# Kernel tuning notes

Measured on AMD Instinct MI355X. Metric: run time of the kernel, lower is better.

Reference implementation:

```python
import jax, jax.numpy as jnp
import numpy as np
import math

B, S, H, E, TOPK, NHEADS = 8, 512, 1024, 8, 2, 8
CAP = int(B * S * 1.5 * TOPK / E)  # 1536


def _linear(x, w, b):
    # torch nn.Linear convention: y = x @ w.T + b, w: [out, in]
    return x @ w.T + b


def _mha(x, in_w, in_b, out_w, out_b, n_heads):
    # torch nn.MultiheadAttention self-attention, eval mode (no dropout)
    Bx, Sx, D = x.shape
    dh = D // n_heads
    qkv = x @ in_w.T + in_b                      # [B,S,3D]
    q, k, v = jnp.split(qkv, 3, axis=-1)
    def heads(t):
        return t.reshape(Bx, Sx, n_heads, dh).transpose(0, 2, 1, 3)  # [B,h,S,dh]
    q, k, v = heads(q), heads(k), heads(v)
    scores = jnp.einsum('bhqd,bhkd->bhqk', q, k) / math.sqrt(dh)
    attn = jax.nn.softmax(scores, axis=-1)
    o = jnp.einsum('bhqk,bhkd->bhqd', attn, v)   # [B,h,S,dh]
    o = o.transpose(0, 2, 1, 3).reshape(Bx, Sx, D)
    return o @ out_w.T + out_b


def setup_inputs() -> dict:
    key = jax.random.key(0)
    ks = jax.random.split(key, 24)
    sc = 0.02
    d = {
        'hidden_states': jax.random.normal(ks[0], (B, S, H), jnp.float32),
        'pos_emb': jax.random.normal(ks[1], (S, H), jnp.float32) * sc,
        'se_w1': jax.random.normal(ks[2], (H // 4, 1), jnp.float32) * sc,
        'se_b1': jnp.zeros((H // 4,), jnp.float32),
        'se_w2': jax.random.normal(ks[3], (H // 4, H // 4), jnp.float32) * sc,
        'se_b2': jnp.zeros((H // 4,), jnp.float32),
        'sexp_w': jax.random.normal(ks[4], (H, H // 4), jnp.float32) * sc,
        'sexp_b': jnp.zeros((H,), jnp.float32),
        'te_w1': jax.random.normal(ks[5], (H, H + 2), jnp.float32) * sc,
        'te_b1': jnp.zeros((H,), jnp.float32),
        'te_w2': jax.random.normal(ks[6], (H, H), jnp.float32) * sc,
        'te_b2': jnp.zeros((H,), jnp.float32),
        'attn_in_w': jax.random.normal(ks[7], (3 * H, H), jnp.float32) * sc,
        'attn_in_b': jnp.zeros((3 * H,), jnp.float32),
        'attn_out_w': jax.random.normal(ks[8], (H, H), jnp.float32) * sc,
        'attn_out_b': jnp.zeros((H,), jnp.float32),
        'tr_w1': jax.random.normal(ks[9], (H, H), jnp.float32) * sc,
        'tr_b1': jnp.zeros((H,), jnp.float32),
        'tr_w2': jax.random.normal(ks[10], (E, H), jnp.float32) * sc,
        'tr_b2': jnp.zeros((E,), jnp.float32),
    }
    return d


def reference(hidden_states, pos_emb, se_w1, se_b1, se_w2, se_b2, sexp_w, sexp_b,
              te_w1, te_b1, te_w2, te_b2, attn_in_w, attn_in_b, attn_out_w, attn_out_b,
              tr_w1, tr_b1, tr_w2, tr_b2):
    b, s, h = hidden_states.shape
    timestamps = jnp.arange(s, dtype=hidden_states.dtype)           # [S]
    seasonality = jnp.sin(timestamps * 2 * jnp.pi / 24)             # [S]
    ts_b = jnp.broadcast_to(timestamps, (b, s))
    se_b = jnp.broadcast_to(seasonality, (b, s))

    position_embeddings = pos_emb[:s][None]                          # [1,S,H]
    seas = jax.nn.relu(_linear(se_b[..., None], se_w1, se_b1))       # [B,S,H/4]
    seas = _linear(seas, se_w2, se_b2)
    seasonal_embeddings = _linear(seas, sexp_w, sexp_b)              # [B,S,H]

    time_features = jnp.stack([ts_b, se_b], axis=-1)                 # [B,S,2]
    combined = jnp.concatenate([hidden_states, time_features], -1)   # [B,S,H+2]
    enc = jax.nn.relu(_linear(combined, te_w1, te_b1))
    enc = _linear(enc, te_w2, te_b2)
    enc = enc + position_embeddings + seasonal_embeddings
    enc = _mha(enc, attn_in_w, attn_in_b, attn_out_w, attn_out_b, NHEADS)

    logits = _linear(jax.nn.relu(_linear(enc, tr_w1, tr_b1)), tr_w2, tr_b2)  # [B,S,E]
    router_probs = jax.nn.softmax(logits, axis=-1)
    top_k_probs, top_k_idx = jax.lax.top_k(router_probs, TOPK)
    top_k_probs = top_k_probs / top_k_probs.sum(-1, keepdims=True)

    capacity = int(b * s * 1.5 * TOPK / E)
    # top-k indices are distinct per token, so summed one-hots replicate the
    # python loop's slot-0 writes exactly.
    onehot = jax.nn.one_hot(top_k_idx, E, dtype=router_probs.dtype)  # [B,S,K,E]
    disp0 = onehot.sum(axis=2)                                        # [B,S,E]
    comb0 = jnp.einsum('bske,bsk->bse', onehot, top_k_probs)          # [B,S,E]
    dispatch = jnp.zeros((b, s, E, capacity), router_probs.dtype).at[:, :, :, 0].set(disp0)
    combine = jnp.zeros((b, s, E, capacity), router_probs.dtype).at[:, :, :, 0].set(comb0)

    p_mean = router_probs.mean(axis=(0, 1))
    aux_loss = jnp.sum(p_mean * jnp.log(p_mean * E + 1e-9))
    return dispatch, combine, router_probs, aux_loss
```

## Files before the change

### kernel.cpp

```cpp
#include <hip/hip_runtime.h>
#include <hip/hip_bf16.h>


#define Hh 1024

typedef __attribute__((ext_vector_type(8))) short short8v;
typedef __attribute__((ext_vector_type(4))) float f32x4;

static __device__ __forceinline__ ushort f2bf(float x) {
  uint u = __float_as_uint(x);
  u += 0x7FFF + ((u >> 16) & 1);
  return (ushort)(u >> 16);
}
static __device__ __forceinline__ float bf2f(ushort h) {
  return __uint_as_float(((uint)h) << 16);
}

template<int EPI, bool RELU, bool HAS_BN, bool HAS_BSN>
__global__ __launch_bounds__(256, 2) void mgemm_k(
    const ushort* __restrict__ A, int lda, long long sAmaj, long long sAmin, int aHi, int aLo,
    const ushort* __restrict__ Bf, int BNT, int BKC, long long sBmaj, long long sBmin,
    float* __restrict__ Cf, ushort* __restrict__ Ch, int ldc, long long sCmaj, long long sCmin,
    int splitOff,
    ushort* __restrict__ pK, ushort* __restrict__ pV,
    int Kd, int zdiv,
    const float* __restrict__ bN, const float* __restrict__ bSN, int ldbs, int smod,
    float alpha)
{
  int gx = gridDim.x, gy = gridDim.y;
  int lin = (blockIdx.z * gy + blockIdx.y) * gx + blockIdx.x;
  int nwg = gx * gy * gridDim.z;
  int cpx = nwg >> 3;
  int swz = (lin & 7) * cpx + (lin >> 3);
  int bz = swz / (gx * gy);
  int rem = swz - bz * (gx * gy);
  int by = rem / gx, bx = rem - by * gx;

  int zj = bz / zdiv, zi = bz - zj * zdiv;
  A += (size_t)zj * sAmaj + (size_t)zi * sAmin;
  const ushort* bfb = Bf + (size_t)zj * sBmaj + (size_t)zi * sBmin;
  long long coff = (long long)zj * sCmaj + (long long)zi * sCmin;

  int m0 = by * 128, n0 = bx * 128;

  __shared__ __align__(16) ushort smem[16384];

  int t = threadIdx.x;
  int l = t & 63, w = t >> 6;
  int wm = w >> 1, wn = w & 1;

  f32x4 acc[4][4];
#pragma unroll
  for (int i = 0; i < 4; ++i)
#pragma unroll
    for (int j = 0; j < 4; ++j) acc[i][j] = (f32x4){0.f, 0.f, 0.f, 0.f};

  int srow = t >> 1;
  int sc = (t & 1) * 2;
  const ushort* gAh = A + (size_t)(m0 + srow) * lda + aHi + sc * 8;
  const ushort* gAl = A + (size_t)(m0 + srow) * lda + aLo + sc * 8;
  int wsw = ((srow >> 1) & 7) << 4;
  int wo0 = (srow * 64 + sc * 16) ^ wsw;
  int wo1 = wo0 ^ 16;

  int aoff[4];
#pragma unroll
  for (int mi = 0; mi < 4; ++mi) {
    int row = wm * 64 + mi * 16 + (l & 15);
    aoff[mi] = (row * 64 + (l >> 4) * 16) ^ (((row >> 1) & 7) << 4);
  }

  const ushort* bph[4];
  const ushort* bpl[4];
  int ntg0 = (n0 >> 4) + wn * 4;
#pragma unroll
  for (int ni = 0; ni < 4; ++ni) {
    bph[ni] = bfb + ((size_t)(ntg0 + ni) * BKC) * 512 + l * 8;
    bpl[ni] = bfb + ((size_t)(BNT + ntg0 + ni) * BKC) * 512 + l * 8;
  }

  int4 a0h0, a0h1, a0l0, a0l1, a1h0, a1h1, a1l0, a1l1;
  short8v B0h[4], B0l[4], B1h[4], B1l[4];

#define LOADA0(s) { a0h0 = *(const int4*)(gAh + (s)*32); a0h1 = *(const int4*)(gAh + (s)*32 + 8); \
                    a0l0 = *(const int4*)(gAl + (s)*32); a0l1 = *(const int4*)(gAl + (s)*32 + 8); }
#define LOADA1(s) { a1h0 = *(const int4*)(gAh + (s)*32); a1h1 = *(const int4*)(gAh + (s)*32 + 8); \
                    a1l0 = *(const int4*)(gAl + (s)*32); a1l1 = *(const int4*)(gAl + (s)*32 + 8); }
#define STOREA(h0, h1, l0, l1, base) { char* nb = (char*)smem + (base); \
    *(int4*)(nb + wo0) = h0; *(int4*)(nb + wo1) = h1; \
    *(int4*)(nb + 8192 + wo0) = l0; *(int4*)(nb + 8192 + wo1) = l1; }
#define LOADB(BH, BL, s) { _Pragma("unroll") \
    for (int ni = 0; ni < 4; ++ni) { \
      BH[ni] = *(const short8v*)(bph[ni] + (size_t)(s) * 512); \
      BL[ni] = *(const short8v*)(bpl[ni] + (size_t)(s) * 512); } }
#define MFMA_STEP(ahb, alb, BH, BL) { \
    short8v ah[4], al[4]; \
    _Pragma("unroll") for (int mi = 0; mi < 4; ++mi) \
      ah[mi] = *(const short8v*)((char*)smem + (ahb) + aoff[mi]); \
    _Pragma("unroll") for (int mi = 0; mi < 4; ++mi) \
      al[mi] = *(const short8v*)((char*)smem + (alb) + aoff[mi]); \
    _Pragma("unroll") for (int ni = 0; ni < 4; ++ni) \
      _Pragma("unroll") for (int mi = 0; mi < 4; ++mi) \
        acc[mi][ni] = __builtin_amdgcn_mfma_f32_16x16x32_bf16(ah[mi], BH[ni], acc[mi][ni], 0, 0, 0); \
    _Pragma("unroll") for (int ni = 0; ni < 4; ++ni) \
      _Pragma("unroll") for (int mi = 0; mi < 4; ++mi) \
        acc[mi][ni] = __builtin_amdgcn_mfma_f32_16x16x32_bf16(al[mi], BH[ni], acc[mi][ni], 0, 0, 0); \
    _Pragma("unroll") for (int ni = 0; ni < 4; ++ni) \
      _Pragma("unroll") for (int mi = 0; mi < 4; ++mi) \
        acc[mi][ni] = __builtin_amdgcn_mfma_f32_16x16x32_bf16(ah[mi], BL[ni], acc[mi][ni], 0, 0, 0); }

  int nt = Kd >> 5;
  LOADA0(0); LOADB(B0h, B0l, 0);
  LOADA1(1); LOADB(B1h, B1l, 1);
  STOREA(a0h0, a0h1, a0l0, a0l1, 0);
  __syncthreads();
  for (int s2 = 0; s2 < nt; s2 += 2) {
    if (s2 + 2 < nt) LOADA0(s2 + 2);
    MFMA_STEP(0, 8192, B0h, B0l);
    if (s2 + 2 < nt) LOADB(B0h, B0l, s2 + 2);
    STOREA(a1h0, a1h1, a1l0, a1l1, 16384);
    __syncthreads();
    if (s2 + 3 < nt) LOADA1(s2 + 3);
    MFMA_STEP(16384, 24576, B1h, B1l);
    if (s2 + 3 < nt) LOADB(B1h, B1l, s2 + 3);
    if (s2 + 2 < nt) STOREA(a0h0, a0h1, a0l0, a0l1, 0);
    __syncthreads();
  }
#undef LOADA0
#undef LOADA1
#undef STOREA
#undef LOADB
#undef MFMA_STEP

#pragma unroll
  for (int mi = 0; mi < 4; ++mi)
#pragma unroll
    for (int j = 0; j < 4; ++j) {
      int m = m0 + wm * 64 + mi * 16 + (l >> 4) * 4 + j;
#pragma unroll
      for (int ni = 0; ni < 4; ++ni) {
        int n = n0 + wn * 64 + ni * 16 + (l & 15);
        float x = acc[mi][ni][j] * alpha;
        if (HAS_BN) x += bN[n];
        if (HAS_BSN) x += bSN[(size_t)(m % smod) * ldbs + n];
        if (RELU) x = fmaxf(x, 0.f);
        acc[mi][ni][j] = x;
      }
    }

  if (EPI == 0) {
    float* Fs = (float*)smem;
#pragma unroll
    for (int p = 0; p < 2; ++p) {
      __syncthreads();
      if (wm == p) {
#pragma unroll
        for (int mi = 0; mi < 4; ++mi)
#pragma unroll
          for (int j = 0; j < 4; ++j) {
            int r = mi * 16 + (l >> 4) * 4 + j;
#pragma unroll
            for (int ni = 0; ni < 4; ++ni) {
              int c = wn * 64 + ni * 16 + (l & 15);
              *(float*)((char*)Fs + ((r * 512 + c * 4) ^ ((r & 7) << 4))) = acc[mi][ni][j];
            }
          }
      }
      __syncthreads();
#pragma unroll
      for (int r8 = 0; r8 < 8; ++r8) {
        int idx = r8 * 256 + t;
        int row = idx >> 5, slot = idx & 31;
        int4 v = *(const int4*)((char*)Fs + ((row * 512 + slot * 16) ^ ((row & 7) << 4)));
        *(int4*)(Cf + coff + (size_t)(m0 + p * 64 + row) * ldc + n0 + slot * 4) = v;
      }
    }
  } else {
    __syncthreads();
    ushort* Es = smem;
    bool isQ = (EPI == 1) || (n0 < 1024);
    bool isK = (EPI == 2) && !isQ && (n0 < 2048);
    int bb = m0 >> 9, s0 = m0 & 511;
    int hh2 = isK ? ((n0 - 1024) >> 7) : ((n0 - 2048) >> 7);
    size_t kvb = (size_t)(bb * 8 + hh2) * 131072;
#pragma unroll
    for (int pass = 0; pass < 2; ++pass) {
      if (isQ) {
#pragma unroll
        for (int mi = 0; mi < 4; ++mi)
#pragma unroll
          for (int j = 0; j < 4; ++j) {
            int lr = wm * 64 + mi * 16 + (l >> 4) * 4 + j;
#pragma unroll
            for (int ni = 0; ni < 4; ++ni) {
              int lcb = (wn * 64 + ni * 16 + (l & 15)) * 2;
              float x = acc[mi][ni][j];
              ushort h = f2bf(x);
              ushort vv = (pass == 0) ? h : f2bf(x - bf2f(h));
              *(ushort*)((char*)Es + ((lr * 256 + lcb) ^ ((lr & 7) << 4))) = vv;
            }
          }
      } else if (isK) {
#pragma unroll
        for (int mi = 0; mi < 4; ++mi)
#pragma unroll
          for (int j = 0; j < 4; ++j) {
            int lr = wm * 64 + mi * 16 + (l >> 4) * 4 + j;
#pragma unroll
            for (int ni = 0; ni < 4; ++ni) {
              int lcb = (wn * 64 + ni * 16 + (l & 15)) * 2;
              float x = acc[mi][ni][j];
              ushort h = f2bf(x);
              ushort vv = (pass == 0) ? h : f2bf(x - bf2f(h));
              *(ushort*)((char*)Es + ((lr * 256 + lcb) ^ ((lr & 7) << 4))) = vv;
            }
          }
      } else {
#pragma unroll
        for (int mi = 0; mi < 4; ++mi)
#pragma unroll
          for (int j = 0; j < 4; ++j) {
            int cc = (wm * 64 + mi * 16 + (l >> 4) * 4 + j) * 2;
#pragma unroll
            for (int ni = 0; ni < 4; ++ni) {
              int rr = wn * 64 + ni * 16 + (l & 15);
              float x = acc[mi][ni][j];
              ushort h = f2bf(x);
              ushort vv = (pass == 0) ? h : f2bf(x - bf2f(h));
              *(ushort*)((char*)Es + ((rr * 256 + cc) ^ ((rr & 7) << 4))) = vv;
            }
          }
      }
      __syncthreads();
      if (isQ) {
        int off = (pass == 0) ? 0 : splitOff;
#pragma unroll
        for (int r = 0; r < 8; ++r) {
          int idx = r * 256 + t;
          int row = idx >> 4, cb = (idx & 15) * 16;
          int4 v = *(const int4*)((char*)Es + ((row * 256 + cb) ^ ((row & 7) << 4)));
          *(int4*)((char*)(Ch + coff + (size_t)(m0 + row) * ldc + off + n0) + cb) = v;
        }
      } else if (isK) {
#pragma unroll
        for (int sw = 0; sw < 8; ++sw) {
          int idx = sw * 256 + t;
          int f = idx >> 6, l2 = idx & 63;
          int st = f >> 2, dc = f & 3;
          int row = st * 16 + (l2 & 15);
          int colB = (dc * 32 + ((l2 >> 4) << 3)) * 2;
          short8v v = *(const short8v*)((char*)Es + ((row * 256 + colB) ^ ((row & 7) << 4)));
          *(short8v*)(pK + kvb + (size_t)((pass * 32 + (s0 >> 4) + st) * 4 + dc) * 512 + l2 * 8) = v;
        }
      } else {
#pragma unroll
        for (int sw = 0; sw < 8; ++sw) {
          int idx = sw * 256 + t;
          int f = idx >> 6, l2 = idx & 63;
          int dt = f >> 2, sch = f & 3;
          int row = dt * 16 + (l2 & 15);
          int colB = (sch * 32 + ((l2 >> 4) << 3)) * 2;
          short8v v = *(const short8v*)((char*)Es + ((row * 256 + colB) ^ ((row & 7) << 4)));
          *(short8v*)(pV + kvb + (size_t)((pass * 8 + dt) * 16 + (s0 >> 5) + sch) * 512 + l2 * 8) = v;
        }
      }
      if (pass == 0) __syncthreads();
    }
  }
}

__global__ __launch_bounds__(64) void convertf_k(
    const float* __restrict__ W, int ldw, ushort* __restrict__ Wf, int NT, int KC)
{
  int kc = blockIdx.x, nt2 = blockIdx.y, l = threadIdx.x;
  const float* src = W + (size_t)(nt2 * 16 + (l & 15)) * ldw + kc * 32 + ((l >> 4) << 3);
  ushort h8[8], l8[8];
#pragma unroll
  for (int j = 0; j < 8; ++j) {
    float x = src[j];
    h8[j] = f2bf(x);
    l8[j] = f2bf(x - bf2f(h8[j]));
  }
  *(int4*)(Wf + ((size_t)nt2 * KC + kc) * 512 + l * 8) = *(int4*)h8;
  *(int4*)(Wf + ((size_t)(NT + nt2) * KC + kc) * 512 + l * 8) = *(int4*)l8;
}

__global__ __launch_bounds__(256) void convert_k(
    const float* __restrict__ W, int lda, ushort* __restrict__ Whl, int K)
{
  int r = blockIdx.x;
  int c = threadIdx.x * 4;
  const float* src = W + (size_t)r * lda + c;
  float x0 = src[0], x1 = src[1], x2 = src[2], x3 = src[3];
  ushort4 h, lo;
  h.x = f2bf(x0); lo.x = f2bf(x0 - bf2f(h.x));
  h.y = f2bf(x1); lo.y = f2bf(x1 - bf2f(h.y));
  h.z = f2bf(x2); lo.z = f2bf(x2 - bf2f(h.z));
  h.w = f2bf(x3); lo.w = f2bf(x3 - bf2f(h.w));
  ushort* dst = Whl + (size_t)r * 2 * K;
  *(ushort4*)&dst[c] = h;
  *(ushort4*)&dst[K + c] = lo;
}

__global__ __launch_bounds__(256) void precompute_k(
    const float* __restrict__ pos_emb,
    const float* __restrict__ se_w1, const float* __restrict__ se_b1,
    const float* __restrict__ se_w2, const float* __restrict__ se_b2,
    const float* __restrict__ sexp_w, const float* __restrict__ sexp_b,
    const float* __restrict__ te_w1, const float* __restrict__ te_b1,
    float* __restrict__ psea, float* __restrict__ bias1)
{
  int s = blockIdx.x, t = threadIdx.x;
  float ts = (float)s;
  float se = sinf(((ts * 2.0f) * 3.14159274101257324f) / 24.0f);
  __shared__ float l1[256], l2[256];
  l1[t] = fmaxf(se * se_w1[t] + se_b1[t], 0.f);
  __syncthreads();
  {
    float a = se_b2[t];
    const float* wr = se_w2 + (size_t)t * 256;
    for (int i = 0; i < 256; ++i) a += l1[i] * wr[i];
    l2[t] = a;
  }
  __syncthreads();
#pragma unroll
  for (int r = 0; r < 4; ++r) {
    int h = r * 256 + t;
    float v = sexp_b[h];
    const float* wr = sexp_w + (size_t)h * 256;
    for (int j = 0; j < 256; ++j) v += l2[j] * wr[j];
    psea[s * Hh + h] = pos_emb[s * Hh + h] + v;
    bias1[s * Hh + h] = te_b1[h] + ts * te_w1[(size_t)h * 1026 + 1024]
                                 + se * te_w1[(size_t)h * 1026 + 1025];
  }
}

__global__ __launch_bounds__(256) void softmax2_k(float* __restrict__ S)
{
  int row = blockIdx.x * 4 + (threadIdx.x >> 6);
  int lane = threadIdx.x & 63;
  float* p = S + (size_t)row * 512;
  float4 a = *(float4*)&p[lane * 4];
  float4 b = *(float4*)&p[256 + lane * 4];
  float m = fmaxf(fmaxf(fmaxf(a.x, a.y), fmaxf(a.z, a.w)),
                  fmaxf(fmaxf(b.x, b.y), fmaxf(b.z, b.w)));
#pragma unroll
  for (int off = 32; off; off >>= 1) m = fmaxf(m, __shfl_xor(m, off));
  a.x = expf(a.x - m); a.y = expf(a.y - m); a.z = expf(a.z - m); a.w = expf(a.w - m);
  b.x = expf(b.x - m); b.y = expf(b.y - m); b.z = expf(b.z - m); b.w = expf(b.w - m);
  float s = a.x + a.y + a.z + a.w + b.x + b.y + b.z + b.w;
#pragma unroll
  for (int off = 32; off; off >>= 1) s += __shfl_xor(s, off);
  float inv = 1.f / s;
  a.x *= inv; a.y *= inv; a.z *= inv; a.w *= inv;
  b.x *= inv; b.y *= inv; b.z *= inv; b.w *= inv;
  ushort* u = (ushort*)S + (size_t)row * 1024;
  ushort4 ha, la, hb, lb;
  ha.x = f2bf(a.x); la.x = f2bf(a.x - bf2f(ha.x));
  ha.y = f2bf(a.y); la.y = f2bf(a.y - bf2f(ha.y));
  ha.z = f2bf(a.z); la.z = f2bf(a.z - bf2f(ha.z));
  ha.w = f2bf(a.w); la.w = f2bf(a.w - bf2f(ha.w));
  hb.x = f2bf(b.x); lb.x = f2bf(b.x - bf2f(hb.x));
  hb.y = f2bf(b.y); lb.y = f2bf(b.y - bf2f(hb.y));
  hb.z = f2bf(b.z); lb.z = f2bf(b.z - bf2f(hb.z));
  hb.w = f2bf(b.w); lb.w = f2bf(b.w - bf2f(hb.w));
  *(ushort4*)&u[lane * 4] = ha;
  *(ushort4*)&u[512 + lane * 4] = la;
  *(ushort4*)&u[256 + lane * 4] = hb;
  *(ushort4*)&u[768 + lane * 4] = lb;
}

__global__ __launch_bounds__(256) void tr2_k(
    const float* __restrict__ h1, const float* __restrict__ w,
    const float* __restrict__ bias, float* __restrict__ logits)
{
  int wid = threadIdx.x >> 6, lane = threadIdx.x & 63;
  int t = blockIdx.x * 4 + wid;
  const float* x = h1 + (size_t)t * Hh;
  float acc[8];
#pragma unroll
  for (int e = 0; e < 8; ++e) acc[e] = 0.f;
  for (int k = lane; k < Hh; k += 64) {
    float xv = x[k];
#pragma unroll
    for (int e = 0; e < 8; ++e) acc[e] += xv * w[e * Hh + k];
  }
#pragma unroll
  for (int e = 0; e < 8; ++e) {
#pragma unroll
    for (int off = 32; off; off >>= 1) acc[e] += __shfl_xor(acc[e], off);
  }
  if (lane == 0) {
#pragma unroll
    for (int e = 0; e < 8; ++e) logits[(size_t)t * 8 + e] = acc[e] + bias[e];
  }
}

__global__ __launch_bounds__(256) void fill0_k(float4* __restrict__ p, long long n4)
{
  long long i = (long long)blockIdx.x * 256 + threadIdx.x;
  long long stride = (long long)gridDim.x * 256;
  float4 z = make_float4(0.f, 0.f, 0.f, 0.f);
  for (; i < n4; i += stride) p[i] = z;
}

__global__ __launch_bounds__(256) void router_k(
    float* __restrict__ out, float* __restrict__ partials)
{
  int t = blockIdx.x * 256 + threadIdx.x;
  float* lg = out + 100663296 + (size_t)t * 8;
  float p[8];
#pragma unroll
  for (int e = 0; e < 8; ++e) p[e] = lg[e];
  float m = p[0];
#pragma unroll
  for (int e = 1; e < 8; ++e) m = fmaxf(m, p[e]);
  float s = 0.f;
#pragma unroll
  for (int e = 0; e < 8; ++e) { p[e] = expf(p[e] - m); s += p[e]; }
  float inv = 1.f / s;
#pragma unroll
  for (int e = 0; e < 8; ++e) p[e] *= inv;
#pragma unroll
  for (int e = 0; e < 8; ++e) lg[e] = p[e];

  int i0 = 0; float v0 = p[0];
#pragma unroll
  for (int e = 1; e < 8; ++e) if (p[e] > v0) { v0 = p[e]; i0 = e; }
  int i1 = -1; float v1 = -1.f;
#pragma unroll
  for (int e = 0; e < 8; ++e) if (e != i0 && p[e] > v1) { v1 = p[e]; i1 = e; }
  float wn = 1.f / (v0 + v1);
  size_t db = (size_t)t * (8 * 1536);
  out[db + (size_t)i0 * 1536] = 1.f;
  out[db + (size_t)i1 * 1536] = 1.f;
  out[50331648 + db + (size_t)i0 * 1536] = v0 * wn;
  out[50331648 + db + (size_t)i1 * 1536] = v1 * wn;

  __shared__ float red[256];
#pragma unroll
  for (int e = 0; e < 8; ++e) {
    red[threadIdx.x] = p[e];
    __syncthreads();
    for (int st = 128; st; st >>= 1) {
      if (threadIdx.x < st) red[threadIdx.x] += red[threadIdx.x + st];
      __syncthreads();
    }
    if (threadIdx.x == 0) partials[blockIdx.x * 8 + e] = red[0];
    __syncthreads();
  }
}

__global__ __launch_bounds__(64) void aux_k(float* __restrict__ partials,
                                            float* __restrict__ out)
{
  int lane = threadIdx.x;
  float v = 0.f;
  if (lane < 8) {
    float s = 0.f;
    for (int b = 0; b < 16; ++b) s += partials[b * 8 + lane];
    float pm = s / 4096.f;
    v = pm * logf(pm * 8.f + 1e-9f);
  }
#pragma unroll
  for (int off = 4; off; off >>= 1) v += __shfl_xor(v, off);
  if (lane == 0) out[100696064] = v;
  partials[lane] = 0.f;
  partials[64 + lane] = 0.f;
}

extern "C" void kernel_launch(void* const* d_in, const int* in_sizes, int n_in,
                              void* d_out, int out_size, void* d_ws, size_t ws_size,
                              hipStream_t stream)
{
  const float* hidden = (const float*)d_in[0];
  const float* pos_emb = (const float*)d_in[1];
  const float* se_w1 = (const float*)d_in[2];
  const float* se_b1 = (const float*)d_in[3];
  const float* se_w2 = (const float*)d_in[4];
  const float* se_b2 = (const float*)d_in[5];
  const float* sexp_w = (const float*)d_in[6];
  const float* sexp_b = (const float*)d_in[7];
  const float* te_w1 = (const float*)d_in[8];
  const float* te_b1 = (const float*)d_in[9];
  const float* te_w2 = (const float*)d_in[10];
  const float* te_b2 = (const float*)d_in[11];
  const float* ain_w = (const float*)d_in[12];
  const float* ain_b = (const float*)d_in[13];
  const float* aout_w = (const float*)d_in[14];
  const float* aout_b = (const float*)d_in[15];
  const float* tr_w1 = (const float*)d_in[16];
  const float* tr_b1 = (const float*)d_in[17];
  const float* tr_w2 = (const float*)d_in[18];
  const float* tr_b2 = (const float*)d_in[19];
  float* out = (float*)d_out;

  char* arena = (char*)d_out;
  ushort* W1f  = (ushort*)(arena + 0);
  ushort* W2f  = (ushort*)(arena + 4194304);
  ushort* Waf  = (ushort*)(arena + 8388608);
  ushort* Wof  = (ushort*)(arena + 20971520);
  ushort* Wtf  = (ushort*)(arena + 25165824);
  ushort* hid2 = (ushort*)(arena + 29360128);
  ushort* enc1 = (ushort*)(arena + 46137344);
  ushort* enc2 = (ushort*)(arena + 62914560);
  ushort* qbuf = (ushort*)(arena + 79691776);
  ushort* Kf   = (ushort*)(arena + 96468992);
  ushort* Vf   = (ushort*)(arena + 113246208);
  float*  scor = (float*)(arena + 130023424);
  ushort* attno= (ushort*)(arena + 197132288);
  ushort* encf = (ushort*)(arena + 213909504);
  float*  h1   = (float*)(arena + 230686720);
  float*  psea = (float*)(arena + 247463936);
  float*  bias1= (float*)(arena + 249561088);
  float*  parts= out + 51380224;
  float*  lgts = out + 100663296;

  convertf_k<<<dim3(32, 64), 64, 0, stream>>>(te_w1, 1026, W1f, 64, 32);
  convertf_k<<<dim3(32, 64), 64, 0, stream>>>(te_w2, 1024, W2f, 64, 32);
  convertf_k<<<dim3(32, 192), 64, 0, stream>>>(ain_w, 1024, Waf, 192, 32);
  convertf_k<<<dim3(32, 64), 64, 0, stream>>>(aout_w, 1024, Wof, 64, 32);
  convertf_k<<<dim3(32, 64), 64, 0, stream>>>(tr_w1, 1024, Wtf, 64, 32);
  convert_k<<<4096, 256, 0, stream>>>(hidden, 1024, hid2, 1024);

  precompute_k<<<512, 256, 0, stream>>>(pos_emb, se_w1, se_b1, se_w2, se_b2,
                                        sexp_w, sexp_b, te_w1, te_b1, psea, bias1);

  mgemm_k<1, true, false, true><<<dim3(8, 32, 1), 256, 0, stream>>>(
      hid2, 2048, 0, 0, 0, 1024,
      W1f, 64, 32, 0, 0,
      nullptr, enc1, 2048, 0, 0, 1024, nullptr, nullptr,
      1024, 1, nullptr, bias1, 1024, 512, 1.f);

  mgemm_k<1, false, true, true><<<dim3(8, 32, 1), 256, 0, stream>>>(
      enc1, 2048, 0, 0, 0, 1024,
      W2f, 64, 32, 0, 0,
      nullptr, enc2, 2048, 0, 0, 1024, nullptr, nullptr,
      1024, 1, te_b2, psea, 1024, 512, 1.f);

  mgemm_k<2, false, true, false><<<dim3(24, 32, 1), 256, 0, stream>>>(
      enc2, 2048, 0, 0, 0, 1024,
      Waf, 192, 32, 0, 0,
      nullptr, qbuf, 2048, 0, 0, 1024, Kf, Vf,
      1024, 1, ain_b, nullptr, 1, 1, 1.f);

  mgemm_k<0, false, false, false><<<dim3(4, 4, 64), 256, 0, stream>>>(
      qbuf, 2048, 1048576, 128, 0, 1024,
      Kf, 32, 4, 1048576, 131072,
      scor, nullptr, 512, 2097152, 262144, 0, nullptr, nullptr,
      128, 8, nullptr, nullptr, 1, 1, 0.08838834764831845f);

  softmax2_k<<<8192, 256, 0, stream>>>(scor);

  mgemm_k<1, false, false, false><<<dim3(1, 4, 64), 256, 0, stream>>>(
      (const ushort*)scor, 1024, 4194304, 524288, 0, 512,
      Vf, 8, 16, 1048576, 131072,
      nullptr, attno, 2048, 1048576, 128, 1024, nullptr, nullptr,
      512, 8, nullptr, nullptr, 1, 1, 1.f);

  mgemm_k<1, false, true, false><<<dim3(8, 32, 1), 256, 0, stream>>>(
      attno, 2048, 0, 0, 0, 1024,
      Wof, 64, 32, 0, 0,
      nullptr, encf, 2048, 0, 0, 1024, nullptr, nullptr,
      1024, 1, aout_b, nullptr, 1, 1, 1.f);

  mgemm_k<0, true, true, false><<<dim3(8, 32, 1), 256, 0, stream>>>(
      encf, 2048, 0, 0, 0, 1024,
      Wtf, 64, 32, 0, 0,
      h1, nullptr, 1024, 0, 0, 0, nullptr, nullptr,
      1024, 1, tr_b1, nullptr, 1, 1, 1.f);

  tr2_k<<<1024, 256, 0, stream>>>(h1, tr_w2, tr_b2, lgts);

  fill0_k<<<4096, 256, 0, stream>>>((float4*)out, 25165824LL);

  router_k<<<16, 256, 0, stream>>>(out, parts);
  aux_k<<<1, 64, 0, stream>>>(parts, out);
}
```

Before: 481.4 us.

## Fuse dispatch zero-fill into GEMM tails, bf16 score output, lighter barriers

Moves the zeroing of the first half of the output (the dispatch tensor region) into the tails of the early GEMM kernels, each block clearing a 128KB slice. The scratch arena is relocated into the combine region so those zero writes do not clobber live data. The fill kernel now only clears the combine half. The QK^T GEMM now writes split bf16 hi/lo scores directly, and softmax reads them, which halves score traffic and drops a float round-trip. GEMM __syncthreads are replaced with an explicit lgkmcnt wait plus s_barrier, which may relax vmem waits but relies on the correct ordering of the global loads.

```diff
diff --git a/kernel.cpp b/kernel.cpp
--- a/kernel.cpp
+++ b/kernel.cpp
@@ -15,6 +15,14 @@
 static __device__ __forceinline__ float bf2f(ushort h) {
   return __uint_as_float(((uint)h) << 16);
 }
+
+#define KBARRIER() do { \
+    __builtin_amdgcn_sched_barrier(0); \
+    asm volatile("s_waitcnt lgkmcnt(0)" ::: "memory"); \
+    __builtin_amdgcn_sched_barrier(0); \
+    __builtin_amdgcn_s_barrier(); \
+    __builtin_amdgcn_sched_barrier(0); \
+  } while (0)
 
 template<int EPI, bool RELU, bool HAS_BN, bool HAS_BSN>
 __global__ __launch_bounds__(256, 2) void mgemm_k(
@@ -25,7 +33,8 @@
     ushort* __restrict__ pK, ushort* __restrict__ pV,
     int Kd, int zdiv,
     const float* __restrict__ bN, const float* __restrict__ bSN, int ldbs, int smod,
-    float alpha)
+    float alpha,
+    char* __restrict__ zout, long long zbase, long long zlimit)
 {
   int gx = gridDim.x, gy = gridDim.y;
   int lin = (blockIdx.z * gy + blockIdx.y) * gx + blockIdx.x;
@@ -113,18 +122,18 @@
   LOADA0(0); LOADB(B0h, B0l, 0);
   LOADA1(1); LOADB(B1h, B1l, 1);
   STOREA(a0h0, a0h1, a0l0, a0l1, 0);
-  __syncthreads();
+  KBARRIER();
   for (int s2 = 0; s2 < nt; s2 += 2) {
     if (s2 + 2 < nt) LOADA0(s2 + 2);
     MFMA_STEP(0, 8192, B0h, B0l);
     if (s2 + 2 < nt) LOADB(B0h, B0l, s2 + 2);
     STOREA(a1h0, a1h1, a1l0, a1l1, 16384);
-    __syncthreads();
+    KBARRIER();
     if (s2 + 3 < nt) LOADA1(s2 + 3);
     MFMA_STEP(16384, 24576, B1h, B1l);
     if (s2 + 3 < nt) LOADB(B1h, B1l, s2 + 3);
     if (s2 + 2 < nt) STOREA(a0h0, a0h1, a0l0, a0l1, 0);
-    __syncthreads();
+    KBARRIER();
   }
 #undef LOADA0
 #undef LOADA1
@@ -267,6 +276,17 @@
       if (pass == 0) __syncthreads();
     }
   }
+
+  if (zlimit > 0) {
+    long long zo = zbase + (long long)lin * 131072LL;
+    if (zo < zlimit) {
+      long long n16 = (zlimit - zo) >> 4;
+      if (n16 > 8192) n16 = 8192;
+      float4* zp = (float4*)(zout + zo);
+      float4 zz = make_float4(0.f, 0.f, 0.f, 0.f);
+      for (long long i = t; i < n16; i += 256) zp[i] = zz;
+    }
+  }
 }
 
 __global__ __launch_bounds__(64) void convertf_k(
@@ -335,39 +355,37 @@
   }
 }
 
-__global__ __launch_bounds__(256) void softmax2_k(float* __restrict__ S)
+__global__ __launch_bounds__(256) void softmax2_k(ushort* __restrict__ S)
 {
   int row = blockIdx.x * 4 + (threadIdx.x >> 6);
   int lane = threadIdx.x & 63;
-  float* p = S + (size_t)row * 512;
-  float4 a = *(float4*)&p[lane * 4];
-  float4 b = *(float4*)&p[256 + lane * 4];
-  float m = fmaxf(fmaxf(fmaxf(a.x, a.y), fmaxf(a.z, a.w)),
-                  fmaxf(fmaxf(b.x, b.y), fmaxf(b.z, b.w)));
+  ushort* u = S + (size_t)row * 1024;
+  int4 hv = *(const int4*)&u[lane * 8];
+  int4 lv = *(const int4*)&u[512 + lane * 8];
+  ushort h8[8], l8[8];
+  *(int4*)h8 = hv; *(int4*)l8 = lv;
+  float x[8];
+#pragma unroll
+  for (int j = 0; j < 8; ++j) x[j] = bf2f(h8[j]) + bf2f(l8[j]);
+  float m = x[0];
+#pragma unroll
+  for (int j = 1; j < 8; ++j) m = fmaxf(m, x[j]);
 #pragma unroll
   for (int off = 32; off; off >>= 1) m = fmaxf(m, __shfl_xor(m, off));
-  a.x = expf(a.x - m); a.y = expf(a.y - m); a.z = expf(a.z - m); a.w = expf(a.w - m);
-  b.x = expf(b.x - m); b.y = expf(b.y - m); b.z = expf(b.z - m); b.w = expf(b.w - m);
-  float s = a.x + a.y + a.z + a.w + b.x + b.y + b.z + b.w;
+  float s = 0.f;
+#pragma unroll
+  for (int j = 0; j < 8; ++j) { x[j] = expf(x[j] - m); s += x[j]; }
 #pragma unroll
   for (int off = 32; off; off >>= 1) s += __shfl_xor(s, off);
   float inv = 1.f / s;
-  a.x *= inv; a.y *= inv; a.z *= inv; a.w *= inv;
-  b.x *= inv; b.y *= inv; b.z *= inv; b.w *= inv;
-  ushort* u = (ushort*)S + (size_t)row * 1024;
-  ushort4 ha, la, hb, lb;
-  ha.x = f2bf(a.x); la.x = f2bf(a.x - bf2f(ha.x));
-  ha.y = f2bf(a.y); la.y = f2bf(a.y - bf2f(ha.y));
-  ha.z = f2bf(a.z); la.z = f2bf(a.z - bf2f(ha.z));
-  ha.w = f2bf(a.w); la.w = f2bf(a.w - bf2f(ha.w));
-  hb.x = f2bf(b.x); lb.x = f2bf(b.x - bf2f(hb.x));
-  hb.y = f2bf(b.y); lb.y = f2bf(b.y - bf2f(hb.y));
-  hb.z = f2bf(b.z); lb.z = f2bf(b.z - bf2f(hb.z));
-  hb.w = f2bf(b.w); lb.w = f2bf(b.w - bf2f(hb.w));
-  *(ushort4*)&u[lane * 4] = ha;
-  *(ushort4*)&u[512 + lane * 4] = la;
-  *(ushort4*)&u[256 + lane * 4] = hb;
-  *(ushort4*)&u[768 + lane * 4] = lb;
+#pragma unroll
+  for (int j = 0; j < 8; ++j) {
+    float p = x[j] * inv;
+    h8[j] = f2bf(p);
+    l8[j] = f2bf(p - bf2f(h8[j]));
+  }
+  *(int4*)&u[lane * 8] = *(int4*)h8;
+  *(int4*)&u[512 + lane * 8] = *(int4*)l8;
 }
 
 __global__ __launch_bounds__(256) void tr2_k(
@@ -494,26 +512,27 @@
   const float* tr_w2 = (const float*)d_in[18];
   const float* tr_b2 = (const float*)d_in[19];
   float* out = (float*)d_out;
-
-  char* arena = (char*)d_out;
-  ushort* W1f  = (ushort*)(arena + 0);
-  ushort* W2f  = (ushort*)(arena + 4194304);
-  ushort* Waf  = (ushort*)(arena + 8388608);
-  ushort* Wof  = (ushort*)(arena + 20971520);
-  ushort* Wtf  = (ushort*)(arena + 25165824);
-  ushort* hid2 = (ushort*)(arena + 29360128);
-  ushort* enc1 = (ushort*)(arena + 46137344);
-  ushort* enc2 = (ushort*)(arena + 62914560);
-  ushort* qbuf = (ushort*)(arena + 79691776);
-  ushort* Kf   = (ushort*)(arena + 96468992);
-  ushort* Vf   = (ushort*)(arena + 113246208);
-  float*  scor = (float*)(arena + 130023424);
-  ushort* attno= (ushort*)(arena + 197132288);
-  ushort* encf = (ushort*)(arena + 213909504);
-  float*  h1   = (float*)(arena + 230686720);
-  float*  psea = (float*)(arena + 247463936);
-  float*  bias1= (float*)(arena + 249561088);
-  float*  parts= out + 51380224;
+  char* ob = (char*)d_out;
+
+  const long long COMB = 201326592LL;
+  ushort* W1f  = (ushort*)(ob + COMB + 0);
+  ushort* W2f  = (ushort*)(ob + COMB + 4194304);
+  ushort* Waf  = (ushort*)(ob + COMB + 8388608);
+  ushort* Wof  = (ushort*)(ob + COMB + 20971520);
+  ushort* Wtf  = (ushort*)(ob + COMB + 25165824);
+  float*  psea = (float*)(ob + COMB + 29360128);
+  float*  bias1= (float*)(ob + COMB + 31457280);
+  ushort* hid2 = (ushort*)(ob + COMB + 33554432);
+  float*  h1   = (float*)(ob + COMB + 33554432);
+  ushort* enc1 = (ushort*)(ob + COMB + 50331648);
+  ushort* attno= (ushort*)(ob + COMB + 50331648);
+  ushort* enc2 = (ushort*)(ob + COMB + 67108864);
+  ushort* encf = (ushort*)(ob + COMB + 67108864);
+  ushort* qbuf = (ushort*)(ob + COMB + 83886080);
+  ushort* Kf   = (ushort*)(ob + COMB + 100663296);
+  ushort* Vf   = (ushort*)(ob + COMB + 117440512);
+  ushort* scorS= (ushort*)(ob + COMB + 134217728);
+  float*  parts= (float*)(ob + COMB + 167772160);
   float*  lgts = out + 100663296;
 
   convertf_k<<<dim3(32, 64), 64, 0, stream>>>(te_w1, 1026, W1f, 64, 32);
@@ -530,49 +549,56 @@
       hid2, 2048, 0, 0, 0, 1024,
       W1f, 64, 32, 0, 0,
       nullptr, enc1, 2048, 0, 0, 1024, nullptr, nullptr,
-      1024, 1, nullptr, bias1, 1024, 512, 1.f);
+      1024, 1, nullptr, bias1, 1024, 512, 1.f,
+      ob, 0LL, 33554432LL);
 
   mgemm_k<1, false, true, true><<<dim3(8, 32, 1), 256, 0, stream>>>(
       enc1, 2048, 0, 0, 0, 1024,
       W2f, 64, 32, 0, 0,
       nullptr, enc2, 2048, 0, 0, 1024, nullptr, nullptr,
-      1024, 1, te_b2, psea, 1024, 512, 1.f);
+      1024, 1, te_b2, psea, 1024, 512, 1.f,
+      ob, 33554432LL, 67108864LL);
 
   mgemm_k<2, false, true, false><<<dim3(24, 32, 1), 256, 0, stream>>>(
       enc2, 2048, 0, 0, 0, 1024,
       Waf, 192, 32, 0, 0,
       nullptr, qbuf, 2048, 0, 0, 1024, Kf, Vf,
-      1024, 1, ain_b, nullptr, 1, 1, 1.f);
-
-  mgemm_k<0, false, false, false><<<dim3(4, 4, 64), 256, 0, stream>>>(
+      1024, 1, ain_b, nullptr, 1, 1, 1.f,
+      ob, 67108864LL, 167772160LL);
+
+  mgemm_k<1, false, false, false><<<dim3(4, 4, 64), 256, 0, stream>>>(
       qbuf, 2048, 1048576, 128, 0, 1024,
       Kf, 32, 4, 1048576, 131072,
-      scor, nullptr, 512, 2097152, 262144, 0, nullptr, nullptr,
-      128, 8, nullptr, nullptr, 1, 1, 0.08838834764831845f);
-
-  softmax2_k<<<8192, 256, 0, stream>>>(scor);
+      nullptr, scorS, 1024, 4194304, 524288, 512, nullptr, nullptr,
+      128, 8, nullptr, nullptr, 1, 1, 0.08838834764831845f,
+      nullptr, 0LL, 0LL);
+
+  softmax2_k<<<8192, 256, 0, stream>>>(scorS);
 
   mgemm_k<1, false, false, false><<<dim3(1, 4, 64), 256, 0, stream>>>(
-      (const ushort*)scor, 1024, 4194304, 524288, 0, 512,
+      scorS, 1024, 4194304, 524288, 0, 512,
       Vf, 8, 16, 1048576, 131072,
       nullptr, attno, 2048, 1048576, 128, 1024, nullptr, nullptr,
-      512, 8, nullptr, nullptr, 1, 1, 1.f);
+      512, 8, nullptr, nullptr, 1, 1, 1.f,
+      nullptr, 0LL, 0LL);
 
   mgemm_k<1, false, true, false><<<dim3(8, 32, 1), 256, 0, stream>>>(
       attno, 2048, 0, 0, 0, 1024,
       Wof, 64, 32, 0, 0,
       nullptr, encf, 2048, 0, 0, 1024, nullptr, nullptr,
-      1024, 1, aout_b, nullptr, 1, 1, 1.f);
+      1024, 1, aout_b, nullptr, 1, 1, 1.f,
+      ob, 167772160LL, 201326592LL);
 
   mgemm_k<0, true, true, false><<<dim3(8, 32, 1), 256, 0, stream>>>(
       encf, 2048, 0, 0, 0, 1024,
       Wtf, 64, 32, 0, 0,
       h1, nullptr, 1024, 0, 0, 0, nullptr, nullptr,
-      1024, 1, tr_b1, nullptr, 1, 1, 1.f);
+      1024, 1, tr_b1, nullptr, 1, 1, 1.f,
+      nullptr, 0LL, 0LL);
 
   tr2_k<<<1024, 256, 0, stream>>>(h1, tr_w2, tr_b2, lgts);
 
-  fill0_k<<<4096, 256, 0, stream>>>((float4*)out, 25165824LL);
+  fill0_k<<<2048, 256, 0, stream>>>((float4*)(out + 50331648), 12582912LL);
 
   router_k<<<16, 256, 0, stream>>>(out, parts);
   aux_k<<<1, 64, 0, stream>>>(parts, out);
```

New measurement: 488.2 us. Within noise of the previous version (+1.4%).

## Use 8-wave 512-thread GEMM blocks and merge weight conversion launches

Applied to the files above, without the earlier changes.

The split-bf16 GEMM moves from 4 waves computing 64x64 sub-tiles each to 8 waves computing 64x32 sub-tiles, with each thread loading one int4 per operand half. This halves per-wave accumulator and B-fragment registers and raises the number of waves per CU for latency hiding. In exchange, each MFMA now needs more LDS A-fragment reads. The five separate weight-conversion launches are also merged into one kernel that selects its source by block index, which saves launch overhead.

```diff
diff --git a/kernel.cpp b/kernel.cpp
--- a/kernel.cpp
+++ b/kernel.cpp
@@ -17,7 +17,7 @@
 }
 
 template<int EPI, bool RELU, bool HAS_BN, bool HAS_BSN>
-__global__ __launch_bounds__(256, 2) void mgemm_k(
+__global__ __launch_bounds__(512, 4) void mgemm_k(
     const ushort* __restrict__ A, int lda, long long sAmaj, long long sAmin, int aHi, int aLo,
     const ushort* __restrict__ Bf, int BNT, int BKC, long long sBmaj, long long sBmin,
     float* __restrict__ Cf, ushort* __restrict__ Ch, int ldc, long long sCmaj, long long sCmin,
@@ -47,21 +47,19 @@
 
   int t = threadIdx.x;
   int l = t & 63, w = t >> 6;
-  int wm = w >> 1, wn = w & 1;
-
-  f32x4 acc[4][4];
+  int wm = w >> 2, wn = w & 3;
+
+  f32x4 acc[4][2];
 #pragma unroll
   for (int i = 0; i < 4; ++i)
 #pragma unroll
-    for (int j = 0; j < 4; ++j) acc[i][j] = (f32x4){0.f, 0.f, 0.f, 0.f};
-
-  int srow = t >> 1;
-  int sc = (t & 1) * 2;
+    for (int j = 0; j < 2; ++j) acc[i][j] = (f32x4){0.f, 0.f, 0.f, 0.f};
+
+  int srow = t >> 2;
+  int sc = t & 3;
   const ushort* gAh = A + (size_t)(m0 + srow) * lda + aHi + sc * 8;
   const ushort* gAl = A + (size_t)(m0 + srow) * lda + aLo + sc * 8;
-  int wsw = ((srow >> 1) & 7) << 4;
-  int wo0 = (srow * 64 + sc * 16) ^ wsw;
-  int wo1 = wo0 ^ 16;
+  int wo = (srow * 64 + sc * 16) ^ (((srow >> 1) & 7) << 4);
 
   int aoff[4];
 #pragma unroll
@@ -70,27 +68,24 @@
     aoff[mi] = (row * 64 + (l >> 4) * 16) ^ (((row >> 1) & 7) << 4);
   }
 
-  const ushort* bph[4];
-  const ushort* bpl[4];
-  int ntg0 = (n0 >> 4) + wn * 4;
-#pragma unroll
-  for (int ni = 0; ni < 4; ++ni) {
+  const ushort* bph[2];
+  const ushort* bpl[2];
+  int ntg0 = (n0 >> 4) + wn * 2;
+#pragma unroll
+  for (int ni = 0; ni < 2; ++ni) {
     bph[ni] = bfb + ((size_t)(ntg0 + ni) * BKC) * 512 + l * 8;
     bpl[ni] = bfb + ((size_t)(BNT + ntg0 + ni) * BKC) * 512 + l * 8;
   }
 
-  int4 a0h0, a0h1, a0l0, a0l1, a1h0, a1h1, a1l0, a1l1;
-  short8v B0h[4], B0l[4], B1h[4], B1l[4];
-
-#define LOADA0(s) { a0h0 = *(const int4*)(gAh + (s)*32); a0h1 = *(const int4*)(gAh + (s)*32 + 8); \
-                    a0l0 = *(const int4*)(gAl + (s)*32); a0l1 = *(const int4*)(gAl + (s)*32 + 8); }
-#define LOADA1(s) { a1h0 = *(const int4*)(gAh + (s)*32); a1h1 = *(const int4*)(gAh + (s)*32 + 8); \
-                    a1l0 = *(const int4*)(gAl + (s)*32); a1l1 = *(const int4*)(gAl + (s)*32 + 8); }
-#define STOREA(h0, h1, l0, l1, base) { char* nb = (char*)smem + (base); \
-    *(int4*)(nb + wo0) = h0; *(int4*)(nb + wo1) = h1; \
-    *(int4*)(nb + 8192 + wo0) = l0; *(int4*)(nb + 8192 + wo1) = l1; }
+  int4 a0h, a0l, a1h, a1l;
+  short8v B0h[2], B0l[2], B1h[2], B1l[2];
+
+#define LOADA0(s) { a0h = *(const int4*)(gAh + (s)*32); a0l = *(const int4*)(gAl + (s)*32); }
+#define LOADA1(s) { a1h = *(const int4*)(gAh + (s)*32); a1l = *(const int4*)(gAl + (s)*32); }
+#define STOREA(h, lo2, base) { char* nb = (char*)smem + (base); \
+    *(int4*)(nb + wo) = h; *(int4*)(nb + 8192 + wo) = lo2; }
 #define LOADB(BH, BL, s) { _Pragma("unroll") \
-    for (int ni = 0; ni < 4; ++ni) { \
+    for (int ni = 0; ni < 2; ++ni) { \
       BH[ni] = *(const short8v*)(bph[ni] + (size_t)(s) * 512); \
       BL[ni] = *(const short8v*)(bpl[ni] + (size_t)(s) * 512); } }
 #define MFMA_STEP(ahb, alb, BH, BL) { \
@@ -99,31 +94,31 @@
       ah[mi] = *(const short8v*)((char*)smem + (ahb) + aoff[mi]); \
     _Pragma("unroll") for (int mi = 0; mi < 4; ++mi) \
       al[mi] = *(const short8v*)((char*)smem + (alb) + aoff[mi]); \
-    _Pragma("unroll") for (int ni = 0; ni < 4; ++ni) \
+    _Pragma("unroll") for (int ni = 0; ni < 2; ++ni) \
       _Pragma("unroll") for (int mi = 0; mi < 4; ++mi) \
         acc[mi][ni] = __builtin_amdgcn_mfma_f32_16x16x32_bf16(ah[mi], BH[ni], acc[mi][ni], 0, 0, 0); \
-    _Pragma("unroll") for (int ni = 0; ni < 4; ++ni) \
+    _Pragma("unroll") for (int ni = 0; ni < 2; ++ni) \
       _Pragma("unroll") for (int mi = 0; mi < 4; ++mi) \
         acc[mi][ni] = __builtin_amdgcn_mfma_f32_16x16x32_bf16(al[mi], BH[ni], acc[mi][ni], 0, 0, 0); \
-    _Pragma("unroll") for (int ni = 0; ni < 4; ++ni) \
+    _Pragma("unroll") for (int ni = 0; ni < 2; ++ni) \
       _Pragma("unroll") for (int mi = 0; mi < 4; ++mi) \
         acc[mi][ni] = __builtin_amdgcn_mfma_f32_16x16x32_bf16(ah[mi], BL[ni], acc[mi][ni], 0, 0, 0); }
 
   int nt = Kd >> 5;
   LOADA0(0); LOADB(B0h, B0l, 0);
   LOADA1(1); LOADB(B1h, B1l, 1);
-  STOREA(a0h0, a0h1, a0l0, a0l1, 0);
+  STOREA(a0h, a0l, 0);
   __syncthreads();
   for (int s2 = 0; s2 < nt; s2 += 2) {
     if (s2 + 2 < nt) LOADA0(s2 + 2);
     MFMA_STEP(0, 8192, B0h, B0l);
     if (s2 + 2 < nt) LOADB(B0h, B0l, s2 + 2);
-    STOREA(a1h0, a1h1, a1l0, a1l1, 16384);
+    STOREA(a1h, a1l, 16384);
     __syncthreads();
     if (s2 + 3 < nt) LOADA1(s2 + 3);
     MFMA_STEP(16384, 24576, B1h, B1l);
     if (s2 + 3 < nt) LOADB(B1h, B1l, s2 + 3);
-    if (s2 + 2 < nt) STOREA(a0h0, a0h1, a0l0, a0l1, 0);
+    if (s2 + 2 < nt) STOREA(a0h, a0l, 0);
     __syncthreads();
   }
 #undef LOADA0
@@ -138,8 +133,8 @@
     for (int j = 0; j < 4; ++j) {
       int m = m0 + wm * 64 + mi * 16 + (l >> 4) * 4 + j;
 #pragma unroll
-      for (int ni = 0; ni < 4; ++ni) {
-        int n = n0 + wn * 64 + ni * 16 + (l & 15);
+      for (int ni = 0; ni < 2; ++ni) {
+        int n = n0 + wn * 32 + ni * 16 + (l & 15);
         float x = acc[mi][ni][j] * alpha;
         if (HAS_BN) x += bN[n];
         if (HAS_BSN) x += bSN[(size_t)(m % smod) * ldbs + n];
@@ -160,16 +155,16 @@
           for (int j = 0; j < 4; ++j) {
             int r = mi * 16 + (l >> 4) * 4 + j;
 #pragma unroll
-            for (int ni = 0; ni < 4; ++ni) {
-              int c = wn * 64 + ni * 16 + (l & 15);
+            for (int ni = 0; ni < 2; ++ni) {
+              int c = wn * 32 + ni * 16 + (l & 15);
               *(float*)((char*)Fs + ((r * 512 + c * 4) ^ ((r & 7) << 4))) = acc[mi][ni][j];
             }
           }
       }
       __syncthreads();
 #pragma unroll
-      for (int r8 = 0; r8 < 8; ++r8) {
-        int idx = r8 * 256 + t;
+      for (int r2 = 0; r2 < 4; ++r2) {
+        int idx = r2 * 512 + t;
         int row = idx >> 5, slot = idx & 31;
         int4 v = *(const int4*)((char*)Fs + ((row * 512 + slot * 16) ^ ((row & 7) << 4)));
         *(int4*)(Cf + coff + (size_t)(m0 + p * 64 + row) * ldc + n0 + slot * 4) = v;
@@ -185,30 +180,15 @@
     size_t kvb = (size_t)(bb * 8 + hh2) * 131072;
 #pragma unroll
     for (int pass = 0; pass < 2; ++pass) {
-      if (isQ) {
+      if (!(EPI == 2 && !isQ && !isK)) {
 #pragma unroll
         for (int mi = 0; mi < 4; ++mi)
 #pragma unroll
           for (int j = 0; j < 4; ++j) {
             int lr = wm * 64 + mi * 16 + (l >> 4) * 4 + j;
 #pragma unroll
-            for (int ni = 0; ni < 4; ++ni) {
-              int lcb = (wn * 64 + ni * 16 + (l & 15)) * 2;
-              float x = acc[mi][ni][j];
-              ushort h = f2bf(x);
-              ushort vv = (pass == 0) ? h : f2bf(x - bf2f(h));
-              *(ushort*)((char*)Es + ((lr * 256 + lcb) ^ ((lr & 7) << 4))) = vv;
-            }
-          }
-      } else if (isK) {
-#pragma unroll
-        for (int mi = 0; mi < 4; ++mi)
-#pragma unroll
-          for (int j = 0; j < 4; ++j) {
-            int lr = wm * 64 + mi * 16 + (l >> 4) * 4 + j;
-#pragma unroll
-            for (int ni = 0; ni < 4; ++ni) {
-              int lcb = (wn * 64 + ni * 16 + (l & 15)) * 2;
+            for (int ni = 0; ni < 2; ++ni) {
+              int lcb = (wn * 32 + ni * 16 + (l & 15)) * 2;
               float x = acc[mi][ni][j];
               ushort h = f2bf(x);
               ushort vv = (pass == 0) ? h : f2bf(x - bf2f(h));
@@ -222,8 +202,8 @@
           for (int j = 0; j < 4; ++j) {
             int cc = (wm * 64 + mi * 16 + (l >> 4) * 4 + j) * 2;
 #pragma unroll
-            for (int ni = 0; ni < 4; ++ni) {
-              int rr = wn * 64 + ni * 16 + (l & 15);
+            for (int ni = 0; ni < 2; ++ni) {
+              int rr = wn * 32 + ni * 16 + (l & 15);
               float x = acc[mi][ni][j];
               ushort h = f2bf(x);
               ushort vv = (pass == 0) ? h : f2bf(x - bf2f(h));
@@ -235,16 +215,16 @@
       if (isQ) {
         int off = (pass == 0) ? 0 : splitOff;
 #pragma unroll
-        for (int r = 0; r < 8; ++r) {
-          int idx = r * 256 + t;
+        for (int r = 0; r < 4; ++r) {
+          int idx = r * 512 + t;
           int row = idx >> 4, cb = (idx & 15) * 16;
           int4 v = *(const int4*)((char*)Es + ((row * 256 + cb) ^ ((row & 7) << 4)));
           *(int4*)((char*)(Ch + coff + (size_t)(m0 + row) * ldc + off + n0) + cb) = v;
         }
       } else if (isK) {
 #pragma unroll
-        for (int sw = 0; sw < 8; ++sw) {
-          int idx = sw * 256 + t;
+        for (int sw = 0; sw < 4; ++sw) {
+          int idx = sw * 512 + t;
           int f = idx >> 6, l2 = idx & 63;
           int st = f >> 2, dc = f & 3;
           int row = st * 16 + (l2 & 15);
@@ -254,8 +234,8 @@
         }
       } else {
 #pragma unroll
-        for (int sw = 0; sw < 8; ++sw) {
-          int idx = sw * 256 + t;
+        for (int sw = 0; sw < 4; ++sw) {
+          int idx = sw * 512 + t;
           int f = idx >> 6, l2 = idx & 63;
           int dt = f >> 2, sch = f & 3;
           int row = dt * 16 + (l2 & 15);
@@ -269,10 +249,18 @@
   }
 }
 
-__global__ __launch_bounds__(64) void convertf_k(
-    const float* __restrict__ W, int ldw, ushort* __restrict__ Wf, int NT, int KC)
-{
-  int kc = blockIdx.x, nt2 = blockIdx.y, l = threadIdx.x;
+__global__ __launch_bounds__(64) void convall_k(
+    const float* __restrict__ te_w1, const float* __restrict__ te_w2,
+    const float* __restrict__ ain_w, const float* __restrict__ aout_w,
+    const float* __restrict__ tr_w1, ushort* __restrict__ base)
+{
+  int kc = blockIdx.x, y = blockIdx.y, l = threadIdx.x;
+  const float* W; int ldw, NT, nt2; ushort* dst;
+  if (y < 64)       { W = te_w1;  ldw = 1026; NT = 64;  nt2 = y;       dst = base; }
+  else if (y < 128) { W = te_w2;  ldw = 1024; NT = 64;  nt2 = y - 64;  dst = base + 2097152; }
+  else if (y < 320) { W = ain_w;  ldw = 1024; NT = 192; nt2 = y - 128; dst = base + 4194304; }
+  else if (y < 384) { W = aout_w; ldw = 1024; NT = 64;  nt2 = y - 320; dst = base + 10485760; }
+  else              { W = tr_w1;  ldw = 1024; NT = 64;  nt2 = y - 384; dst = base + 12582912; }
   const float* src = W + (size_t)(nt2 * 16 + (l & 15)) * ldw + kc * 32 + ((l >> 4) << 3);
   ushort h8[8], l8[8];
 #pragma unroll
@@ -281,8 +269,8 @@
     h8[j] = f2bf(x);
     l8[j] = f2bf(x - bf2f(h8[j]));
   }
-  *(int4*)(Wf + ((size_t)nt2 * KC + kc) * 512 + l * 8) = *(int4*)h8;
-  *(int4*)(Wf + ((size_t)(NT + nt2) * KC + kc) * 512 + l * 8) = *(int4*)l8;
+  *(int4*)(dst + ((size_t)nt2 * 32 + kc) * 512 + l * 8) = *(int4*)h8;
+  *(int4*)(dst + ((size_t)(NT + nt2) * 32 + kc) * 512 + l * 8) = *(int4*)l8;
 }
 
 __global__ __launch_bounds__(256) void convert_k(
@@ -496,11 +484,7 @@
   float* out = (float*)d_out;
 
   char* arena = (char*)d_out;
-  ushort* W1f  = (ushort*)(arena + 0);
-  ushort* W2f  = (ushort*)(arena + 4194304);
-  ushort* Waf  = (ushort*)(arena + 8388608);
-  ushort* Wof  = (ushort*)(arena + 20971520);
-  ushort* Wtf  = (ushort*)(arena + 25165824);
+  ushort* Wbase= (ushort*)(arena + 0);
   ushort* hid2 = (ushort*)(arena + 29360128);
   ushort* enc1 = (ushort*)(arena + 46137344);
   ushort* enc2 = (ushort*)(arena + 62914560);
@@ -516,35 +500,30 @@
   float*  parts= out + 51380224;
   float*  lgts = out + 100663296;
 
-  convertf_k<<<dim3(32, 64), 64, 0, stream>>>(te_w1, 1026, W1f, 64, 32);
-  convertf_k<<<dim3(32, 64), 64, 0, stream>>>(te_w2, 1024, W2f, 64, 32);
-  convertf_k<<<dim3(32, 192), 64, 0, stream>>>(ain_w, 1024, Waf, 192, 32);
-  convertf_k<<<dim3(32, 64), 64, 0, stream>>>(aout_w, 1024, Wof, 64, 32);
-  convertf_k<<<dim3(32, 64), 64, 0, stream>>>(tr_w1, 1024, Wtf, 64, 32);
+  convall_k<<<dim3(32, 448), 64, 0, stream>>>(te_w1, te_w2, ain_w, aout_w, tr_w1, Wbase);
   convert_k<<<4096, 256, 0, stream>>>(hidden, 1024, hid2, 1024);
-
   precompute_k<<<512, 256, 0, stream>>>(pos_emb, se_w1, se_b1, se_w2, se_b2,
                                         sexp_w, sexp_b, te_w1, te_b1, psea, bias1);
 
-  mgemm_k<1, true, false, true><<<dim3(8, 32, 1), 256, 0, stream>>>(
+  mgemm_k<1, true, false, true><<<dim3(8, 32, 1), 512, 0, stream>>>(
       hid2, 2048, 0, 0, 0, 1024,
-      W1f, 64, 32, 0, 0,
+      Wbase, 64, 32, 0, 0,
       nullptr, enc1, 2048, 0, 0, 1024, nullptr, nullptr,
       1024, 1, nullptr, bias1, 1024, 512, 1.f);
 
-  mgemm_k<1, false, true, true><<<dim3(8, 32, 1), 256, 0, stream>>>(
+  mgemm_k<1, false, true, true><<<dim3(8, 32, 1), 512, 0, stream>>>(
       enc1, 2048, 0, 0, 0, 1024,
-      W2f, 64, 32, 0, 0,
+      Wbase + 2097152, 64, 32, 0, 0,
       nullptr, enc2, 2048, 0, 0, 1024, nullptr, nullptr,
       1024, 1, te_b2, psea, 1024, 512, 1.f);
 
-  mgemm_k<2, false, true, false><<<dim3(24, 32, 1), 256, 0, stream>>>(
+  mgemm_k<2, false, true, false><<<dim3(24, 32, 1), 512, 0, stream>>>(
       enc2, 2048, 0, 0, 0, 1024,
-      Waf, 192, 32, 0, 0,
+      Wbase + 4194304, 192, 32, 0, 0,
       nullptr, qbuf, 2048, 0, 0, 1024, Kf, Vf,
       1024, 1, ain_b, nullptr, 1, 1, 1.f);
 
-  mgemm_k<0, false, false, false><<<dim3(4, 4, 64), 256, 0, stream>>>(
+  mgemm_k<0, false, false, false><<<dim3(4, 4, 64), 512, 0, stream>>>(
       qbuf, 2048, 1048576, 128, 0, 1024,
       Kf, 32, 4, 1048576, 131072,
       scor, nullptr, 512, 2097152, 262144, 0, nullptr, nullptr,
@@ -552,21 +531,21 @@
 
   softmax2_k<<<8192, 256, 0, stream>>>(scor);
 
-  mgemm_k<1, false, false, false><<<dim3(1, 4, 64), 256, 0, stream>>>(
+  mgemm_k<1, false, false, false><<<dim3(1, 4, 64), 512, 0, stream>>>(
       (const ushort*)scor, 1024, 4194304, 524288, 0, 512,
       Vf, 8, 16, 1048576, 131072,
       nullptr, attno, 2048, 1048576, 128, 1024, nullptr, nullptr,
       512, 8, nullptr, nullptr, 1, 1, 1.f);
 
-  mgemm_k<1, false, true, false><<<dim3(8, 32, 1), 256, 0, stream>>>(
+  mgemm_k<1, false, true, false><<<dim3(8, 32, 1), 512, 0, stream>>>(
       attno, 2048, 0, 0, 0, 1024,
-      Wof, 64, 32, 0, 0,
+      Wbase + 10485760, 64, 32, 0, 0,
       nullptr, encf, 2048, 0, 0, 1024, nullptr, nullptr,
       1024, 1, aout_b, nullptr, 1, 1, 1.f);
 
-  mgemm_k<0, true, true, false><<<dim3(8, 32, 1), 256, 0, stream>>>(
+  mgemm_k<0, true, true, false><<<dim3(8, 32, 1), 512, 0, stream>>>(
       encf, 2048, 0, 0, 0, 1024,
-      Wtf, 64, 32, 0, 0,
+      Wbase + 12582912, 64, 32, 0, 0,
       h1, nullptr, 1024, 0, 0, 0, nullptr, nullptr,
       1024, 1, tr_b1, nullptr, 1, 1, 1.f);
 
```

Result: slower. 537.4 us (+11.6%).
